# Performance work log

Hardware: AMD Instinct MI355X
Metric: run time of the kernel (lower is better)

The kernel has to match this reference:

```python
import jax, jax.numpy as jnp
import numpy as np

N_NODES = 100_000
N_EDGES = 1_600_000  # avg degree 16
D_FEAT = 64


def setup_inputs() -> dict:
    key = jax.random.key(0)
    k_x, k_val, k_src, k_dst = jax.random.split(key, 4)
    x = jax.random.normal(k_x, (N_NODES, D_FEAT), dtype=jnp.float32)
    edge_val = jax.random.uniform(k_val, (N_EDGES,), dtype=jnp.float32)
    edge_src = jax.random.randint(k_src, (N_EDGES,), 0, N_NODES, dtype=jnp.int32)
    edge_dst = jax.random.randint(k_dst, (N_EDGES,), 0, N_NODES, dtype=jnp.int32)
    return {"x": x, "edge_val": edge_val, "edge_src": edge_src, "edge_dst": edge_dst}


def reference(x, edge_val, edge_src, edge_dst):
    # out = adj @ x  with adj in COO form:
    # out[dst] += val * x[src]   (sparse-dense matmul, SpMM)
    msgs = x[edge_src] * edge_val[:, None]          # [E, D] gather + scale
    out = jax.ops.segment_sum(msgs, edge_dst, num_segments=N_NODES)  # [N, D] scatter-add
    return out
```

## Files before the change

kernel.cpp:

```cpp
#include <hip/hip_runtime.h>

#define N_NODES 100000
#define N_EDGES 1600000
#define D_FEAT 64
#define NPB 128
#define K_BUCKETS 782
#define CAP 2304
#define A_BLOCKS 400
#define A_CHUNK 4000

__global__ void scatterA(const int* __restrict__ src, const int* __restrict__ dst,
                         const float* __restrict__ val, int* __restrict__ cursor,
                         int2* __restrict__ bdata) {
    __shared__ int sh_cnt[K_BUCKETS];
    __shared__ int sh_base[K_BUCKETS];
    for (int i = threadIdx.x; i < K_BUCKETS; i += 256) sh_cnt[i] = 0;
    __syncthreads();
    const int base = blockIdx.x * A_CHUNK;
    for (int j = threadIdx.x; j < A_CHUNK; j += 256)
        atomicAdd(&sh_cnt[dst[base + j] >> 7], 1);
    __syncthreads();
    for (int i = threadIdx.x; i < K_BUCKETS; i += 256) {
        const int c = sh_cnt[i];
        sh_base[i] = c ? (i * CAP + atomicAdd(&cursor[i], c)) : 0;
    }
    __syncthreads();
    for (int i = threadIdx.x; i < K_BUCKETS; i += 256) sh_cnt[i] = 0;
    __syncthreads();
    for (int j = threadIdx.x; j < A_CHUNK; j += 256) {
        const int e = base + j;
        const int d = dst[e];
        const int b = d >> 7;
        const int slot = atomicAdd(&sh_cnt[b], 1);
        bdata[sh_base[b] + slot] =
            make_int2(src[e] | ((d & 127) << 17), __float_as_int(val[e]));
    }
}

__global__ void sortB(int2* __restrict__ bdata, const int* __restrict__ cursor,
                      int* __restrict__ rbeg, int* __restrict__ rdeg) {
    __shared__ int2 sh_e[CAP];
    __shared__ int cnt[NPB];
    __shared__ int cur[NPB];
    const int b = blockIdx.x;
    const int count = min(cursor[b], CAP);
    const int base = b * CAP;
    const int t = threadIdx.x;
    if (t < NPB) cnt[t] = 0;
    __syncthreads();
    for (int j = t; j < count; j += 256) {
        const int2 e = bdata[base + j];
        sh_e[j] = e;
        atomicAdd(&cnt[e.x >> 17], 1);
    }
    __syncthreads();
    const int v = (t < NPB) ? cnt[t] : 0;
    for (int off = 1; off < NPB; off <<= 1) {
        int u = 0;
        if (t < NPB && t >= off) u = cnt[t - off];
        __syncthreads();
        if (t < NPB) cnt[t] += u;
        __syncthreads();
    }
    const int row0 = b * NPB;
    if (t < NPB) {
        const int excl = cnt[t] - v;
        cur[t] = excl;
        if (row0 + t < N_NODES) { rbeg[row0 + t] = base + excl; rdeg[row0 + t] = v; }
    }
    __syncthreads();
    for (int j = t; j < count; j += 256) {
        const int2 pv = sh_e[j];
        const int dl = pv.x >> 17;
        const int slot = atomicAdd(&cur[dl], 1);
        bdata[base + slot] = make_int2(pv.x & 0x1FFFF, pv.y);
    }
}

__global__ void spmm_csr(const float* __restrict__ x,
                         const int* __restrict__ rbeg,
                         const int* __restrict__ rdeg,
                         const int2* __restrict__ csr,
                         float* __restrict__ out) {
    const int tid = blockIdx.x * blockDim.x + threadIdx.x;
    const int row = tid >> 4;
    const int c = tid & 15;
    if (row >= N_NODES) return;
    const int beg = rbeg[row];
    const int end = beg + rdeg[row];
    float4 acc = {0.f, 0.f, 0.f, 0.f};
    int j = beg;
    for (; j + 2 <= end; j += 2) {
        const int2 p0 = csr[j];
        const int2 p1 = csr[j + 1];
        const float4 m0 = ((const float4*)(x + (size_t)p0.x * D_FEAT))[c];
        const float4 m1 = ((const float4*)(x + (size_t)p1.x * D_FEAT))[c];
        const float v0 = __int_as_float(p0.y);
        const float v1 = __int_as_float(p1.y);
        acc.x += v0 * m0.x + v1 * m1.x;
        acc.y += v0 * m0.y + v1 * m1.y;
        acc.z += v0 * m0.z + v1 * m1.z;
        acc.w += v0 * m0.w + v1 * m1.w;
    }
    if (j < end) {
        const int2 p0 = csr[j];
        const float4 m0 = ((const float4*)(x + (size_t)p0.x * D_FEAT))[c];
        const float v0 = __int_as_float(p0.y);
        acc.x += v0 * m0.x;
        acc.y += v0 * m0.y;
        acc.z += v0 * m0.z;
        acc.w += v0 * m0.w;
    }
    ((float4*)(out + (size_t)row * D_FEAT))[c] = acc;
}

extern "C" void kernel_launch(void* const* d_in, const int* in_sizes, int n_in,
                              void* d_out, int out_size, void* d_ws, size_t ws_size,
                              hipStream_t stream) {
    const float* x        = (const float*)d_in[0];
    const float* edge_val = (const float*)d_in[1];
    const int*   edge_src = (const int*)d_in[2];
    const int*   edge_dst = (const int*)d_in[3];
    float* out = (float*)d_out;

    int* ws     = (int*)d_ws;
    int* cursor = ws;
    int* rbeg   = cursor + K_BUCKETS;
    int* rdeg   = rbeg + N_NODES;
    size_t used = (size_t)K_BUCKETS + 2 * N_NODES;
    used = (used + 1) & ~(size_t)1;
    int2* bdata = (int2*)(ws + used);

    hipMemsetAsync(cursor, 0, K_BUCKETS * sizeof(int), stream);

    const int B = 256;
    const int gridRow = (N_NODES * 16 + B - 1) / B;

    scatterA<<<A_BLOCKS, 256, 0, stream>>>(edge_src, edge_dst, edge_val, cursor, bdata);
    sortB   <<<K_BUCKETS, 256, 0, stream>>>(bdata, cursor, rbeg, rdeg);
    spmm_csr<<<gridRow, B, 0, stream>>>(x, rbeg, rdeg, bdata, out);
}
```

Measured before the change: 191.5 us.

## Fuse prep stages into cooperative kernel and gather fp16 features in SpMM

Replaces the memset, scatter and bucket-sort kernels with a single cooperative kernel that uses grid syncs, and uses the spare blocks during the scatter phase to convert x to fp16. The SpMM kernel then gathers half-precision rows, halving gather bytes, and unrolls the edge loop by four. This cuts launch overhead and gather bandwidth, but rounds features to fp16, which may exceed tolerance, and adds the conversion pass plus grid-sync costs.

```diff
diff --git a/kernel.cpp b/kernel.cpp
--- a/kernel.cpp
+++ b/kernel.cpp
@@ -1,4 +1,8 @@
 #include <hip/hip_runtime.h>
+#include <hip/hip_fp16.h>
+#include <hip/hip_cooperative_groups.h>
+
+namespace cg = cooperative_groups;
 
 #define N_NODES 100000
 #define N_EDGES 1600000
@@ -6,110 +10,154 @@
 #define NPB 128
 #define K_BUCKETS 782
 #define CAP 2304
-#define A_BLOCKS 400
+#define SCAT_BLOCKS 400
 #define A_CHUNK 4000
+#define PREP_GRID 768
 
-__global__ void scatterA(const int* __restrict__ src, const int* __restrict__ dst,
-                         const float* __restrict__ val, int* __restrict__ cursor,
-                         int2* __restrict__ bdata) {
-    __shared__ int sh_cnt[K_BUCKETS];
-    __shared__ int sh_base[K_BUCKETS];
-    for (int i = threadIdx.x; i < K_BUCKETS; i += 256) sh_cnt[i] = 0;
-    __syncthreads();
-    const int base = blockIdx.x * A_CHUNK;
-    for (int j = threadIdx.x; j < A_CHUNK; j += 256)
-        atomicAdd(&sh_cnt[dst[base + j] >> 7], 1);
-    __syncthreads();
-    for (int i = threadIdx.x; i < K_BUCKETS; i += 256) {
-        const int c = sh_cnt[i];
-        sh_base[i] = c ? (i * CAP + atomicAdd(&cursor[i], c)) : 0;
+__global__ __launch_bounds__(256)
+void prep(const float* __restrict__ x,
+          const int* __restrict__ src, const int* __restrict__ dst,
+          const float* __restrict__ val,
+          int* __restrict__ cursor, int2* __restrict__ bdata,
+          __half* __restrict__ xh,
+          int* __restrict__ rbeg, int* __restrict__ rdeg) {
+    cg::grid_group grid = cg::this_grid();
+    __shared__ int smem[4864];
+    const int t = threadIdx.x;
+    const int blk = blockIdx.x;
+
+    {
+        const int gid = blk * 256 + t;
+        if (gid < K_BUCKETS) cursor[gid] = 0;
     }
-    __syncthreads();
-    for (int i = threadIdx.x; i < K_BUCKETS; i += 256) sh_cnt[i] = 0;
-    __syncthreads();
-    for (int j = threadIdx.x; j < A_CHUNK; j += 256) {
-        const int e = base + j;
-        const int d = dst[e];
-        const int b = d >> 7;
-        const int slot = atomicAdd(&sh_cnt[b], 1);
-        bdata[sh_base[b] + slot] =
-            make_int2(src[e] | ((d & 127) << 17), __float_as_int(val[e]));
+    __threadfence();
+    grid.sync();
+
+    if (blk < SCAT_BLOCKS) {
+        int* sh_cnt  = smem;
+        int* sh_base = smem + K_BUCKETS;
+        for (int i = t; i < K_BUCKETS; i += 256) sh_cnt[i] = 0;
+        __syncthreads();
+        const int base = blk * A_CHUNK;
+        for (int j = t; j < A_CHUNK; j += 256)
+            atomicAdd(&sh_cnt[dst[base + j] >> 7], 1);
+        __syncthreads();
+        for (int i = t; i < K_BUCKETS; i += 256) {
+            const int c = sh_cnt[i];
+            sh_base[i] = c ? (i * CAP + atomicAdd(&cursor[i], c)) : 0;
+        }
+        __syncthreads();
+        for (int i = t; i < K_BUCKETS; i += 256) sh_cnt[i] = 0;
+        __syncthreads();
+        for (int j = t; j < A_CHUNK; j += 256) {
+            const int e = base + j;
+            const int d = dst[e];
+            const int b = d >> 7;
+            const int slot = atomicAdd(&sh_cnt[b], 1);
+            bdata[sh_base[b] + slot] =
+                make_int2(src[e] | ((d & 127) << 17), __float_as_int(val[e]));
+        }
+    } else {
+        const float4* xv = (const float4*)x;
+        uint2* xo = (uint2*)xh;
+        const int nth = (PREP_GRID - SCAT_BLOCKS) * 256;
+        const int total4 = N_NODES * D_FEAT / 4;
+        for (int i = (blk - SCAT_BLOCKS) * 256 + t; i < total4; i += nth) {
+            const float4 f = xv[i];
+            const __half2 a = __floats2half2_rn(f.x, f.y);
+            const __half2 b = __floats2half2_rn(f.z, f.w);
+            xo[i] = make_uint2(*(const unsigned int*)&a, *(const unsigned int*)&b);
+        }
+    }
+    __threadfence();
+    grid.sync();
+
+    int2* sh_e = (int2*)smem;
+    int*  cnt  = smem + 4608;
+    int*  cur  = smem + 4736;
+    for (int b = blk; b < K_BUCKETS; b += PREP_GRID) {
+        const int count = min(cursor[b], CAP);
+        const int base = b * CAP;
+        if (t < NPB) cnt[t] = 0;
+        __syncthreads();
+        for (int j = t; j < count; j += 256) {
+            const int2 e = bdata[base + j];
+            sh_e[j] = e;
+            atomicAdd(&cnt[e.x >> 17], 1);
+        }
+        __syncthreads();
+        const int v = (t < NPB) ? cnt[t] : 0;
+        for (int off = 1; off < NPB; off <<= 1) {
+            int u = 0;
+            if (t < NPB && t >= off) u = cnt[t - off];
+            __syncthreads();
+            if (t < NPB) cnt[t] += u;
+            __syncthreads();
+        }
+        const int row0 = b * NPB;
+        if (t < NPB) {
+            const int excl = cnt[t] - v;
+            cur[t] = excl;
+            if (row0 + t < N_NODES) { rbeg[row0 + t] = base + excl; rdeg[row0 + t] = v; }
+        }
+        __syncthreads();
+        for (int j = t; j < count; j += 256) {
+            const int2 pv = sh_e[j];
+            const int dl = pv.x >> 17;
+            const int slot = atomicAdd(&cur[dl], 1);
+            bdata[base + slot] = make_int2(pv.x & 0x1FFFF, pv.y);
+        }
+        __syncthreads();
     }
 }
 
-__global__ void sortB(int2* __restrict__ bdata, const int* __restrict__ cursor,
-                      int* __restrict__ rbeg, int* __restrict__ rdeg) {
-    __shared__ int2 sh_e[CAP];
-    __shared__ int cnt[NPB];
-    __shared__ int cur[NPB];
-    const int b = blockIdx.x;
-    const int count = min(cursor[b], CAP);
-    const int base = b * CAP;
-    const int t = threadIdx.x;
-    if (t < NPB) cnt[t] = 0;
-    __syncthreads();
-    for (int j = t; j < count; j += 256) {
-        const int2 e = bdata[base + j];
-        sh_e[j] = e;
-        atomicAdd(&cnt[e.x >> 17], 1);
-    }
-    __syncthreads();
-    const int v = (t < NPB) ? cnt[t] : 0;
-    for (int off = 1; off < NPB; off <<= 1) {
-        int u = 0;
-        if (t < NPB && t >= off) u = cnt[t - off];
-        __syncthreads();
-        if (t < NPB) cnt[t] += u;
-        __syncthreads();
-    }
-    const int row0 = b * NPB;
-    if (t < NPB) {
-        const int excl = cnt[t] - v;
-        cur[t] = excl;
-        if (row0 + t < N_NODES) { rbeg[row0 + t] = base + excl; rdeg[row0 + t] = v; }
-    }
-    __syncthreads();
-    for (int j = t; j < count; j += 256) {
-        const int2 pv = sh_e[j];
-        const int dl = pv.x >> 17;
-        const int slot = atomicAdd(&cur[dl], 1);
-        bdata[base + slot] = make_int2(pv.x & 0x1FFFF, pv.y);
-    }
-}
-
-__global__ void spmm_csr(const float* __restrict__ x,
-                         const int* __restrict__ rbeg,
-                         const int* __restrict__ rdeg,
-                         const int2* __restrict__ csr,
-                         float* __restrict__ out) {
+__global__ void spmm_half(const __half* __restrict__ xh,
+                          const int* __restrict__ rbeg,
+                          const int* __restrict__ rdeg,
+                          const int2* __restrict__ csr,
+                          float* __restrict__ out) {
     const int tid = blockIdx.x * blockDim.x + threadIdx.x;
     const int row = tid >> 4;
     const int c = tid & 15;
     if (row >= N_NODES) return;
     const int beg = rbeg[row];
-    const int end = beg + rdeg[row];
+    const int deg = rdeg[row];
+    const int end = beg + deg;
     float4 acc = {0.f, 0.f, 0.f, 0.f};
     int j = beg;
-    for (; j + 2 <= end; j += 2) {
+    const int end4 = beg + (deg & ~3);
+    for (; j < end4; j += 4) {
         const int2 p0 = csr[j];
         const int2 p1 = csr[j + 1];
-        const float4 m0 = ((const float4*)(x + (size_t)p0.x * D_FEAT))[c];
-        const float4 m1 = ((const float4*)(x + (size_t)p1.x * D_FEAT))[c];
+        const int2 p2 = csr[j + 2];
+        const int2 p3 = csr[j + 3];
+        const uint2 r0 = ((const uint2*)(xh + (size_t)p0.x * D_FEAT))[c];
+        const uint2 r1 = ((const uint2*)(xh + (size_t)p1.x * D_FEAT))[c];
+        const uint2 r2 = ((const uint2*)(xh + (size_t)p2.x * D_FEAT))[c];
+        const uint2 r3 = ((const uint2*)(xh + (size_t)p3.x * D_FEAT))[c];
         const float v0 = __int_as_float(p0.y);
         const float v1 = __int_as_float(p1.y);
-        acc.x += v0 * m0.x + v1 * m1.x;
-        acc.y += v0 * m0.y + v1 * m1.y;
-        acc.z += v0 * m0.z + v1 * m1.z;
-        acc.w += v0 * m0.w + v1 * m1.w;
+        const float v2 = __int_as_float(p2.y);
+        const float v3 = __int_as_float(p3.y);
+        float2 a0 = __half22float2(*(const __half2*)&r0.x), b0 = __half22float2(*(const __half2*)&r0.y);
+        float2 a1 = __half22float2(*(const __half2*)&r1.x), b1 = __half22float2(*(const __half2*)&r1.y);
+        float2 a2 = __half22float2(*(const __half2*)&r2.x), b2 = __half22float2(*(const __half2*)&r2.y);
+        float2 a3 = __half22float2(*(const __half2*)&r3.x), b3 = __half22float2(*(const __half2*)&r3.y);
+        acc.x += v0 * a0.x + v1 * a1.x + v2 * a2.x + v3 * a3.x;
+        acc.y += v0 * a0.y + v1 * a1.y + v2 * a2.y + v3 * a3.y;
+        acc.z += v0 * b0.x + v1 * b1.x + v2 * b2.x + v3 * b3.x;
+        acc.w += v0 * b0.y + v1 * b1.y + v2 * b2.y + v3 * b3.y;
     }
-    if (j < end) {
+    for (; j < end; ++j) {
         const int2 p0 = csr[j];
-        const float4 m0 = ((const float4*)(x + (size_t)p0.x * D_FEAT))[c];
+        const uint2 r0 = ((const uint2*)(xh + (size_t)p0.x * D_FEAT))[c];
         const float v0 = __int_as_float(p0.y);
-        acc.x += v0 * m0.x;
-        acc.y += v0 * m0.y;
-        acc.z += v0 * m0.z;
-        acc.w += v0 * m0.w;
+        const float2 a0 = __half22float2(*(const __half2*)&r0.x);
+        const float2 b0 = __half22float2(*(const __half2*)&r0.y);
+        acc.x += v0 * a0.x;
+        acc.y += v0 * a0.y;
+        acc.z += v0 * b0.x;
+        acc.w += v0 * b0.y;
     }
     ((float4*)(out + (size_t)row * D_FEAT))[c] = acc;
 }
@@ -130,13 +178,13 @@
     size_t used = (size_t)K_BUCKETS + 2 * N_NODES;
     used = (used + 1) & ~(size_t)1;
     int2* bdata = (int2*)(ws + used);
+    __half* xh  = (__half*)(bdata + (size_t)K_BUCKETS * CAP);
 
-    hipMemsetAsync(cursor, 0, K_BUCKETS * sizeof(int), stream);
+    void* args[] = { (void*)&x, (void*)&edge_src, (void*)&edge_dst, (void*)&edge_val,
+                     (void*)&cursor, (void*)&bdata, (void*)&xh, (void*)&rbeg, (void*)&rdeg };
+    hipLaunchCooperativeKernel((void*)prep, dim3(PREP_GRID), dim3(256), args, 0, stream);
 
     const int B = 256;
     const int gridRow = (N_NODES * 16 + B - 1) / B;
-
-    scatterA<<<A_BLOCKS, 256, 0, stream>>>(edge_src, edge_dst, edge_val, cursor, bdata);
-    sortB   <<<K_BUCKETS, 256, 0, stream>>>(bdata, cursor, rbeg, rdeg);
-    spmm_csr<<<gridRow, B, 0, stream>>>(x, rbeg, rdeg, bdata, out);
+    spmm_half<<<gridRow, B, 0, stream>>>(xh, rbeg, rdeg, bdata, out);
 }
```

After: 459.4 us. 2.4x slower.
